# Kernel tuning notes

Measured on AMD Instinct MI355X. Metric: run time of the kernel, lower is better.

Reference implementation:

```python
import jax, jax.numpy as jnp
import numpy as np

B, S, D_IN, D_OUT, H = 4, 2048, 1024, 1024, 16
HD = D_OUT // H  # 64


def setup_inputs() -> dict:
    key = jax.random.key(0)
    ks = jax.random.split(key, 6)
    s = 1.0 / np.sqrt(D_IN)
    return {
        "x": jax.random.normal(ks[0], (B, S, D_IN), dtype=jnp.float32),
        "Wq": jax.random.uniform(ks[1], (D_IN, D_OUT), jnp.float32, -s, s),
        "Wk": jax.random.uniform(ks[2], (D_IN, D_OUT), jnp.float32, -s, s),
        "Wv": jax.random.uniform(ks[3], (D_IN, D_OUT), jnp.float32, -s, s),
        "Wo": jax.random.uniform(ks[4], (D_OUT, D_OUT), jnp.float32, -s, s),
        "bo": jax.random.uniform(ks[5], (D_OUT,), jnp.float32, -s, s),
    }


def reference(x, Wq, Wk, Wv, Wo, bo):
    b, s, _ = x.shape
    # QKV projections -> [b, H, s, hd]
    def split_heads(t):
        return t.reshape(b, s, H, HD).transpose(0, 2, 1, 3)
    q = split_heads(x @ Wq)
    k = split_heads(x @ Wk)
    v = split_heads(x @ Wv)
    # attention scores [b, H, s, s]
    scores = jnp.einsum("bhqd,bhkd->bhqk", q, k)
    causal = jnp.triu(jnp.ones((s, s), dtype=bool), k=1)
    scores = jnp.where(causal, -jnp.inf, scores)
    attn = jax.nn.softmax(scores / np.sqrt(HD), axis=-1)
    ctx = jnp.einsum("bhqk,bhkd->bhqd", attn, v)
    ctx = ctx.transpose(0, 2, 1, 3).reshape(b, s, D_OUT)
    return ctx @ Wo + bo
```

## Files before the change

kernel.cpp:

```cpp
#include <hip/hip_runtime.h>

typedef __attribute__((ext_vector_type(8))) short bf16x8;
typedef __attribute__((ext_vector_type(4))) float f32x4;
typedef __attribute__((ext_vector_type(4))) unsigned uint4v;

#define SM_C 0.18033688011112042f
#define SM_M 20.0f
#define MFMA16 __builtin_amdgcn_mfma_f32_16x16x32_bf16

__device__ __forceinline__ unsigned short f2bf(float f) {
  unsigned u = __builtin_bit_cast(unsigned, f);
  u += 0x7fffu + ((u >> 16) & 1u);
  return (unsigned short)(u >> 16);
}

__device__ __forceinline__ unsigned cvtpk(float lo, float hi) {
  unsigned r;
  asm volatile("v_cvt_pk_bf16_f32 %0, %1, %2" : "=v"(r) : "v"(lo), "v"(hi));
  return r;
}

__device__ __forceinline__ void gload16(const void* g, void* lds) {
  __builtin_amdgcn_global_load_lds(
      (const __attribute__((address_space(1))) void*)g,
      (__attribute__((address_space(3))) void*)lds, 16, 0, 0);
}

#define BARRIER __builtin_amdgcn_s_barrier()
#define LGKM0 asm volatile("s_waitcnt lgkmcnt(0)" ::: "memory")

__global__ __launch_bounds__(256) void cvt_x(const float* __restrict__ in,
                                             unsigned short* __restrict__ out,
                                             int n4) {
  int i = blockIdx.x * 256 + threadIdx.x;
  int stride = gridDim.x * 256;
  for (; i < n4; i += stride) {
    float4 v = ((const float4*)in)[i];
    unsigned short o0 = f2bf(v.x), o1 = f2bf(v.y), o2 = f2bf(v.z), o3 = f2bf(v.w);
    unsigned long long packed = (unsigned long long)o0 | ((unsigned long long)o1 << 16) |
                                ((unsigned long long)o2 << 32) | ((unsigned long long)o3 << 48);
    ((unsigned long long*)out)[i] = packed;
  }
}

__global__ __launch_bounds__(256) void transpose_w4(const float* __restrict__ W0,
                                                    const float* __restrict__ W1,
                                                    const float* __restrict__ W2,
                                                    const float* __restrict__ W3,
                                                    unsigned short* __restrict__ WT) {
  __shared__ float tile[32][33];
  const int z = blockIdx.z;
  const float* W = (z == 0) ? W0 : (z == 1) ? W1 : (z == 2) ? W2 : W3;
  unsigned short* WTo = WT + (size_t)z * 1048576;
  int bx = blockIdx.x, by = blockIdx.y;
  int x = bx * 32 + threadIdx.x;
  for (int i = 0; i < 4; ++i) {
    int r = threadIdx.y + i * 8;
    tile[r][threadIdx.x] = W[(by * 32 + r) * 1024 + x];
  }
  __syncthreads();
  int nx = by * 32 + threadIdx.x;
  for (int i = 0; i < 4; ++i) {
    int r = threadIdx.y + i * 8;
    WTo[(long)(bx * 32 + r) * 1024 + nx] = f2bf(tile[threadIdx.x][r]);
  }
}

template <int NR, int MODE>
__global__ __launch_bounds__(512, 1) void gemm3b(const unsigned short* __restrict__ A,
                                                 const unsigned short* __restrict__ BT,
                                                 unsigned short* __restrict__ Cb,
                                                 float* __restrict__ Cf,
                                                 const float* __restrict__ bias,
                                                 int M, int N, int K) {
  constexpr int BN = NR * 64;
  __shared__ alignas(16) unsigned short As[3][256 * 64];
  __shared__ alignas(16) unsigned short Bs[2][BN * 64];

  const int nbn = N / BN;
  const int tmg = (M / 256) / 8;
  const int cc = blockIdx.x >> 3, xc = blockIdx.x & 7;
  const int tm = xc * tmg + cc / nbn, tn = cc % nbn;

  const int t = threadIdx.x, l = t & 63, wid = t >> 6;
  const int wm = wid >> 2, wn = wid & 3;
  const int lr = l & 15, lg = l >> 4;

  f32x4 acc[8][NR] = {};

  const int sq = t >> 3;
  const int sslot8 = ((t & 7) ^ (sq & 7)) * 8;
  const unsigned short* Ath = A + ((long)tm * 256 + sq) * K + sslot8;
  const unsigned short* Bth = BT + ((long)tn * BN + sq) * K + sslot8;
  const int ldsoff = sq * 64 + (t & 7) * 8;

#define STGA(buf, q, kt) \
  gload16(Ath + (long)((q)*64) * K + (kt)*64, &As[buf][(q)*4096 + ldsoff])
#define STGB(buf, u, kt) \
  gload16(Bth + (long)((u)*64) * K + (kt)*64, &Bs[buf][(u)*4096 + ldsoff])

  const int NT = K >> 6;
#pragma unroll
  for (int q = 0; q < 4; ++q) STGA(0, q, 0);
#pragma unroll
  for (int u = 0; u < NR; ++u) STGB(0, u, 0);
#pragma unroll
  for (int q = 0; q < 4; ++q) STGA(1, q, 1);

  const int offk0 = (lg ^ (lr & 7)) * 8;
  const int offk1 = ((4 + lg) ^ (lr & 7)) * 8;
  const int arow0 = (wm * 128 + lr) * 64;
  const int brow0 = (wn * (NR * 16) + lr) * 64;

#define DS_A(MH)                                                   \
  _Pragma("unroll") for (int m_ = 0; m_ < 4; ++m_) {               \
    const unsigned short* ap_ = Ac + arow0 + ((MH)*4 + m_) * 1024; \
    af[m_][0] = *(const bf16x8*)(ap_ + offk0);                     \
    af[m_][1] = *(const bf16x8*)(ap_ + offk1);                     \
  }
#define DS_B_ALL                                          \
  _Pragma("unroll") for (int n_ = 0; n_ < NR; ++n_) {     \
    const unsigned short* bp_ = Bc + brow0 + n_ * 1024;   \
    bfr[n_][0] = *(const bf16x8*)(bp_ + offk0);           \
    bfr[n_][1] = *(const bf16x8*)(bp_ + offk1);           \
  }
#define MM(MH)                                                              \
  __builtin_amdgcn_s_setprio(1);                                            \
  _Pragma("unroll") for (int m_ = 0; m_ < 4; ++m_)                          \
  _Pragma("unroll") for (int n_ = 0; n_ < NR; ++n_) {                       \
    acc[(MH)*4 + m_][n_] = MFMA16(af[m_][0], bfr[n_][0],                    \
                                  acc[(MH)*4 + m_][n_], 0, 0, 0);           \
    acc[(MH)*4 + m_][n_] = MFMA16(af[m_][1], bfr[n_][1],                    \
                                  acc[(MH)*4 + m_][n_], 0, 0, 0);           \
  }                                                                         \
  __builtin_amdgcn_s_setprio(0);

  int cur3 = 0;
  int stg3 = 2;
  for (int tt = 0; tt < NT; ++tt) {
    const unsigned short* Ac = As[cur3];
    const unsigned short* Bc = Bs[tt & 1];

    bf16x8 af[4][2];
    bf16x8 bfr[NR][2];

    if (tt == NT - 1) asm volatile("s_waitcnt vmcnt(0)" ::: "memory");
    else              asm volatile("s_waitcnt vmcnt(4)" ::: "memory");
    BARRIER;
    DS_A(0);
    DS_B_ALL;
    if (tt + 1 < NT) {
      const int nbB = (tt + 1) & 1;
#pragma unroll
      for (int u = 0; u < NR; ++u) STGB(nbB, u, tt + 1);
    }
    BARRIER;
    LGKM0;
    MM(0);

    DS_A(1);
    if (tt + 2 < NT) {
#pragma unroll
      for (int q = 0; q < 4; ++q) STGA(stg3, q, tt + 2);
    }
    BARRIER;
    LGKM0;
    MM(1);

    cur3 = (cur3 == 2) ? 0 : cur3 + 1;
    stg3 = (stg3 == 2) ? 0 : stg3 + 1;
  }
#undef DS_A
#undef DS_B_ALL
#undef MM
#undef STGA
#undef STGB

  const long crow = (long)tm * 256 + wm * 128;
  const int ccol = tn * BN + wn * (NR * 16);

  if constexpr (MODE == 1) {
#pragma unroll
    for (int m = 0; m < 8; ++m)
#pragma unroll
      for (int n = 0; n < NR; ++n)
#pragma unroll
        for (int r = 0; r < 4; ++r) {
          long row = crow + m * 16 + lg * 4 + r;
          int col = ccol + n * 16 + lr;
          Cf[row * N + col] = acc[m][n][r] + bias[col];
        }
  } else {
#pragma unroll
    for (int n = 0; n < NR; ++n) {
      const int colg = ccol + n * 16;
      const int plane = colg >> 10;
      if (plane < 2) {
        unsigned short* pl = Cb + (size_t)plane * 8388608;
        const int pc = (colg & 1023) + lr;
#pragma unroll
        for (int m = 0; m < 8; ++m)
#pragma unroll
          for (int r = 0; r < 4; ++r) {
            long row = crow + m * 16 + lg * 4 + r;
            pl[row * 1024 + pc] = f2bf(acc[m][n][r]);
          }
      } else {
        unsigned short* VtW = Cb + 16777216;
        const int bq = (tm >> 3) << 4;
        const int sbase = ((tm & 7) << 8) + wm * 128;
        const int vcol = (colg & 1023) + lr;
        const long vtrow = (long)(bq + (vcol >> 6)) * 64 + (vcol & 63);
#pragma unroll
        for (int m = 0; m < 8; ++m) {
          const int srow_ = sbase + m * 16 + lg * 4;
          const int lwb = srow_ & 63;
          const int stt = srow_ >> 6;
          const int vp0 = (lwb & 32) | (((lwb >> 2) & 3) << 3) | (((lwb >> 4) & 1) << 2);
          unsigned long long pk4 =
              (unsigned long long)f2bf(acc[m][n][0]) |
              ((unsigned long long)f2bf(acc[m][n][1]) << 16) |
              ((unsigned long long)f2bf(acc[m][n][2]) << 32) |
              ((unsigned long long)f2bf(acc[m][n][3]) << 48);
          *(unsigned long long*)(VtW + vtrow * 2048 + stt * 64 + vp0) = pk4;
        }
      }
    }
  }
}

template <int TWO>
__device__ __forceinline__ void attn_tile(
    const unsigned short* __restrict__ Kc, const unsigned short* __restrict__ Vc,
    int lr, int lg, bool mask0, bool mask1, int kv0, int q0row, int q1row,
    const bf16x8 (&qf)[2][2], f32x4 (&cacc)[2][4], float (&l_r)[2]) {
  constexpr int S0 = TWO ? 0 : 1;
  f32x4 p[2][4];
#pragma unroll
  for (int s = S0; s < 2; ++s)
#pragma unroll
    for (int g = 0; g < 4; ++g) p[s][g] = f32x4{0.f, 0.f, 0.f, 0.f};

  __builtin_amdgcn_s_setprio(1);
#pragma unroll
  for (int g = 0; g < 4; ++g) {
    const int key = g * 16 + lr;
    const int swz = (key & 7) << 3;
#pragma unroll
    for (int c = 0; c < 2; ++c) {
      bf16x8 kf = *(const bf16x8*)(Kc + key * 64 + ((c * 32 + lg * 8) ^ swz));
#pragma unroll
      for (int s = S0; s < 2; ++s)
        p[s][g] = MFMA16(kf, qf[s][c], p[s][g], 0, 0, 0);
    }
  }
  __builtin_amdgcn_s_setprio(0);

  if (TWO && mask0) {
#pragma unroll
    for (int g = 0; g < 4; ++g)
#pragma unroll
      for (int r = 0; r < 4; ++r)
        if (kv0 + g * 16 + lg * 4 + r > q0row) p[0][g][r] = -1e30f;
  }
  if (mask1) {
#pragma unroll
    for (int g = 0; g < 4; ++g)
#pragma unroll
      for (int r = 0; r < 4; ++r)
        if (kv0 + g * 16 + lg * 4 + r > q1row) p[1][g][r] = -1e30f;
  }

  const float SM_NMC = -SM_M * SM_C;
  unsigned pk[2][4][2];
#pragma unroll
  for (int s = S0; s < 2; ++s) {
    float e[4][4];
#pragma unroll
    for (int g = 0; g < 4; ++g)
#pragma unroll
      for (int r = 0; r < 4; ++r)
        e[g][r] = __builtin_amdgcn_exp2f(__builtin_fmaf(p[s][g][r], SM_C, SM_NMC));
    float t0 = (e[0][0] + e[0][1]) + (e[0][2] + e[0][3]);
    float t1 = (e[1][0] + e[1][1]) + (e[1][2] + e[1][3]);
    float t2 = (e[2][0] + e[2][1]) + (e[2][2] + e[2][3]);
    float t3 = (e[3][0] + e[3][1]) + (e[3][2] + e[3][3]);
    l_r[s] += (t0 + t1) + (t2 + t3);
#pragma unroll
    for (int g = 0; g < 4; ++g) {
      pk[s][g][0] = cvtpk(e[g][0], e[g][1]);
      pk[s][g][1] = cvtpk(e[g][2], e[g][3]);
    }
  }

#pragma unroll
  for (int sl = 0; sl < 2; ++sl) {
    bf16x8 vf[4];
#pragma unroll
    for (int n = 0; n < 4; ++n) {
      const int hd = n * 16 + lr;
      vf[n] = *(const bf16x8*)(Vc + hd * 64 + ((sl * 32 + lg * 8) ^ ((hd & 7) << 3)));
    }
    __builtin_amdgcn_s_setprio(1);
#pragma unroll
    for (int s = S0; s < 2; ++s) {
      uint4v pw = {pk[s][2 * sl][0], pk[s][2 * sl][1], pk[s][2 * sl + 1][0], pk[s][2 * sl + 1][1]};
      bf16x8 pa = __builtin_bit_cast(bf16x8, pw);
#pragma unroll
      for (int n = 0; n < 4; ++n)
        cacc[s][n] = MFMA16(pa, vf[n], cacc[s][n], 0, 0, 0);
    }
    __builtin_amdgcn_s_setprio(0);
  }
}

__global__ __launch_bounds__(256, 4) void flash_attn(const unsigned short* __restrict__ Qp,
                                                     const unsigned short* __restrict__ Kp,
                                                     const unsigned short* __restrict__ Vt,
                                                     unsigned short* __restrict__ Ctx) {
  __shared__ alignas(16) unsigned short Ks[2][64 * 64];
  __shared__ alignas(16) unsigned short Vs[2][64 * 64];
  const int bid = blockIdx.x;
  const int qt = bid >> 6;
  const int bh = bid & 63;
  const int b = bh >> 4, h = bh & 15;
  const int t = threadIdx.x, l = t & 63, w = t >> 6;
  const int lr = l & 15, lg = l >> 4;
  const long rowbase = (long)b * 2048;
  const int colbase = h * 64;
  const int q0 = qt * 64 + w * 16;
  const int q1 = (31 - qt) * 64 + w * 16;
  const int q0row = q0 + lr, q1row = q1 + lr;
  const int nkv = 32 - qt;

  bf16x8 qf[2][2];
#pragma unroll
  for (int c = 0; c < 2; ++c) {
    qf[0][c] = *(const bf16x8*)(Qp + (rowbase + q0 + lr) * 1024 + colbase + c * 32 + lg * 8);
    qf[1][c] = *(const bf16x8*)(Qp + (rowbase + q1 + lr) * 1024 + colbase + c * 32 + lg * 8);
  }

  f32x4 cacc[2][4];
  float l_r[2];
#pragma unroll
  for (int s = 0; s < 2; ++s) {
    l_r[s] = 0.f;
#pragma unroll
    for (int n = 0; n < 4; ++n) cacc[s][n] = f32x4{0.f, 0.f, 0.f, 0.f};
  }

  const int srow = w * 16 + (l >> 3);
  const int scol = (l & 7) * 8;
  const int kswz = scol ^ ((srow & 7) << 3);
  const unsigned short* kp = Kp + (rowbase + srow) * 1024 + colbase + kswz;
  const unsigned short* vp = Vt + ((long)(bh * 64 + srow)) * 2048 + kswz;
  unsigned short* ksd0 = &Ks[0][(w * 16) * 64];
  unsigned short* vsd0 = &Vs[0][(w * 16) * 64];

#define STAGE(buf)                                    \
  do {                                                \
    gload16(kp, ksd0 + (buf) * 4096);                 \
    gload16(kp + 8 * 1024, ksd0 + (buf) * 4096 + 512);\
    gload16(vp, vsd0 + (buf) * 4096);                 \
    gload16(vp + 8 * 2048, vsd0 + (buf) * 4096 + 512);\
    kp += 64 * 1024;                                  \
    vp += 64;                                         \
  } while (0)

#define TILE_WAIT(j)                                                          \
  do {                                                                        \
    if ((j) == nkv - 1) asm volatile("s_waitcnt vmcnt(0)" ::: "memory");      \
    else                asm volatile("s_waitcnt vmcnt(4)" ::: "memory");      \
    asm volatile("s_barrier" ::: "memory");                                   \
  } while (0)

  STAGE(0);
  STAGE(1);

  int j = 0;
  for (; j <= qt; ++j) {
    const int cur = j & 1;
    TILE_WAIT(j);
    attn_tile<1>(Ks[cur], Vs[cur], lr, lg, j == qt, false, j * 64, q0row, q1row,
                 qf, cacc, l_r);
    asm volatile("s_barrier" ::: "memory");
    if (j + 2 < nkv) STAGE(cur);
  }
  for (; j < nkv; ++j) {
    const int cur = j & 1;
    TILE_WAIT(j);
    attn_tile<0>(Ks[cur], Vs[cur], lr, lg, false, j == nkv - 1, j * 64, q0row, q1row,
                 qf, cacc, l_r);
    asm volatile("s_barrier" ::: "memory");
    if (j + 2 < nkv) STAGE(cur);
  }
#undef STAGE
#undef TILE_WAIT

#pragma unroll
  for (int s = 0; s < 2; ++s) {
    float rs = l_r[s];
    rs += __shfl_xor(rs, 16);
    rs += __shfl_xor(rs, 32);
    float invl = 1.f / rs;
    float ilq[4];
#pragma unroll
    for (int r = 0; r < 4; ++r) ilq[r] = __shfl(invl, lg * 20 + r);
    const int qs = (s == 0) ? q0 : q1;
#pragma unroll
    for (int n = 0; n < 4; ++n)
#pragma unroll
      for (int r = 0; r < 4; ++r) {
        long row = rowbase + qs + lg * 4 + r;
        Ctx[row * 1024 + colbase + n * 16 + lr] = f2bf(cacc[s][n][r] * ilq[r]);
      }
  }
}

extern "C" void kernel_launch(void* const* d_in, const int* in_sizes, int n_in,
                              void* d_out, int out_size, void* d_ws, size_t ws_size,
                              hipStream_t stream) {
  (void)in_sizes; (void)n_in; (void)out_size; (void)ws_size;
  const float* x  = (const float*)d_in[0];
  const float* Wq = (const float*)d_in[1];
  const float* Wk = (const float*)d_in[2];
  const float* Wv = (const float*)d_in[3];
  const float* Wo = (const float*)d_in[4];
  const float* bo = (const float*)d_in[5];
  float* out = (float*)d_out;

  unsigned short* ws = (unsigned short*)d_ws;
  unsigned short* xb  = ws;
  unsigned short* WqT = ws + 8388608;
  unsigned short* WoT = WqT + 3145728;
  unsigned short* QKV = WqT + 4194304;
  unsigned short* Qp  = QKV;
  unsigned short* Kp  = QKV + 8388608;
  unsigned short* Vt  = QKV + 16777216;
  unsigned short* Ctx = QKV + 25165824;

  cvt_x<<<2048, 256, 0, stream>>>(x, xb, 8192 * 1024 / 4);

  dim3 tb(32, 8), tg(32, 32, 4);
  transpose_w4<<<tg, tb, 0, stream>>>(Wq, Wk, Wv, Wo, WqT);

  gemm3b<3, 0><<<512, 512, 0, stream>>>(xb, WqT, QKV, nullptr, nullptr,
                                        8192, 3072, 1024);

  flash_attn<<<1024, 256, 0, stream>>>(Qp, Kp, Vt, Ctx);

  gemm3b<2, 1><<<256, 512, 0, stream>>>(Ctx, WoT, nullptr, out, bo,
                                        8192, 1024, 1024);
}
```

Before: 138.6 us.

## Replace 256-row triple-buffered GEMM with 128x128 double-buffered tiles; fuse prep kernels

Merges the x-conversion and weight-transpose kernels into one launch to cut a kernel launch. Replaces the 512-thread 256xBN GEMM that used a 3-stage A buffer and split MFMA phases with a simpler 256-thread 128x128 tile kernel using double buffering and one barrier per k-step. This gives more blocks and higher occupancy, but the smaller tiles mean less data reuse per block. The simpler pipeline also exposes more load latency, since it waits on vmcnt(0) every iteration.

After: 148.3 us, median of 2. 7.0% more time.

```diff
diff --git a/kernel.cpp b/kernel.cpp
--- a/kernel.cpp
+++ b/kernel.cpp
@@ -28,195 +28,174 @@
 
 #define BARRIER __builtin_amdgcn_s_barrier()
 #define LGKM0 asm volatile("s_waitcnt lgkmcnt(0)" ::: "memory")
-
-__global__ __launch_bounds__(256) void cvt_x(const float* __restrict__ in,
-                                             unsigned short* __restrict__ out,
-                                             int n4) {
-  int i = blockIdx.x * 256 + threadIdx.x;
-  int stride = gridDim.x * 256;
-  for (; i < n4; i += stride) {
-    float4 v = ((const float4*)in)[i];
-    unsigned short o0 = f2bf(v.x), o1 = f2bf(v.y), o2 = f2bf(v.z), o3 = f2bf(v.w);
-    unsigned long long packed = (unsigned long long)o0 | ((unsigned long long)o1 << 16) |
-                                ((unsigned long long)o2 << 32) | ((unsigned long long)o3 << 48);
-    ((unsigned long long*)out)[i] = packed;
-  }
-}
-
-__global__ __launch_bounds__(256) void transpose_w4(const float* __restrict__ W0,
-                                                    const float* __restrict__ W1,
-                                                    const float* __restrict__ W2,
-                                                    const float* __restrict__ W3,
-                                                    unsigned short* __restrict__ WT) {
+#define VM0 asm volatile("s_waitcnt vmcnt(0)" ::: "memory")
+
+__global__ __launch_bounds__(256) void prep(const float* __restrict__ x,
+                                            unsigned short* __restrict__ xb,
+                                            const float* __restrict__ W0,
+                                            const float* __restrict__ W1,
+                                            const float* __restrict__ W2,
+                                            const float* __restrict__ W3,
+                                            unsigned short* __restrict__ WT) {
   __shared__ float tile[32][33];
-  const int z = blockIdx.z;
-  const float* W = (z == 0) ? W0 : (z == 1) ? W1 : (z == 2) ? W2 : W3;
-  unsigned short* WTo = WT + (size_t)z * 1048576;
-  int bx = blockIdx.x, by = blockIdx.y;
-  int x = bx * 32 + threadIdx.x;
-  for (int i = 0; i < 4; ++i) {
-    int r = threadIdx.y + i * 8;
-    tile[r][threadIdx.x] = W[(by * 32 + r) * 1024 + x];
-  }
-  __syncthreads();
-  int nx = by * 32 + threadIdx.x;
-  for (int i = 0; i < 4; ++i) {
-    int r = threadIdx.y + i * 8;
-    WTo[(long)(bx * 32 + r) * 1024 + nx] = f2bf(tile[threadIdx.x][r]);
-  }
-}
-
-template <int NR, int MODE>
-__global__ __launch_bounds__(512, 1) void gemm3b(const unsigned short* __restrict__ A,
-                                                 const unsigned short* __restrict__ BT,
-                                                 unsigned short* __restrict__ Cb,
-                                                 float* __restrict__ Cf,
-                                                 const float* __restrict__ bias,
-                                                 int M, int N, int K) {
-  constexpr int BN = NR * 64;
-  __shared__ alignas(16) unsigned short As[3][256 * 64];
-  __shared__ alignas(16) unsigned short Bs[2][BN * 64];
-
-  const int nbn = N / BN;
-  const int tmg = (M / 256) / 8;
+  const int bid = blockIdx.x;
+  if (bid < 2048) {
+    int i = bid * 256 + threadIdx.x;
+    for (; i < 2097152; i += 2048 * 256) {
+      float4 v = ((const float4*)x)[i];
+      unsigned long long packed = (unsigned long long)f2bf(v.x) |
+                                  ((unsigned long long)f2bf(v.y) << 16) |
+                                  ((unsigned long long)f2bf(v.z) << 32) |
+                                  ((unsigned long long)f2bf(v.w) << 48);
+      ((unsigned long long*)xb)[i] = packed;
+    }
+  } else {
+    int b2 = bid - 2048;
+    const int z = b2 >> 10;
+    b2 &= 1023;
+    const int bx = b2 & 31, by = b2 >> 5;
+    const float* W = (z == 0) ? W0 : (z == 1) ? W1 : (z == 2) ? W2 : W3;
+    unsigned short* WTo = WT + (size_t)z * 1048576;
+    const int tx = threadIdx.x & 31, ty = threadIdx.x >> 5;
+    const int xcol = bx * 32 + tx;
+    for (int i = 0; i < 4; ++i) {
+      int r = ty + i * 8;
+      tile[r][tx] = W[(by * 32 + r) * 1024 + xcol];
+    }
+    __syncthreads();
+    const int nx = by * 32 + tx;
+    for (int i = 0; i < 4; ++i) {
+      int r = ty + i * 8;
+      WTo[(long)(bx * 32 + r) * 1024 + nx] = f2bf(tile[tx][r]);
+    }
+  }
+}
+
+template <int MODE>
+__global__ __launch_bounds__(256) void gemm97(const unsigned short* __restrict__ A,
+                                              const unsigned short* __restrict__ BT,
+                                              unsigned short* __restrict__ Cb,
+                                              float* __restrict__ Cf,
+                                              const float* __restrict__ bias,
+                                              int M, int N, int K) {
+  __shared__ alignas(16) unsigned short As[2][128 * 64];
+  __shared__ alignas(16) unsigned short Bs[2][128 * 64];
+
+  const int nbn = N >> 7;
+  const int tmg = (M >> 7) >> 3;
   const int cc = blockIdx.x >> 3, xc = blockIdx.x & 7;
   const int tm = xc * tmg + cc / nbn, tn = cc % nbn;
 
   const int t = threadIdx.x, l = t & 63, wid = t >> 6;
-  const int wm = wid >> 2, wn = wid & 3;
+  const int wm = wid >> 1, wn = wid & 1;
   const int lr = l & 15, lg = l >> 4;
 
-  f32x4 acc[8][NR] = {};
+  f32x4 acc[4][4] = {};
 
   const int sq = t >> 3;
   const int sslot8 = ((t & 7) ^ (sq & 7)) * 8;
-  const unsigned short* Ath = A + ((long)tm * 256 + sq) * K + sslot8;
-  const unsigned short* Bth = BT + ((long)tn * BN + sq) * K + sslot8;
+  const unsigned short* Ath = A + ((long)tm * 128 + sq) * K + sslot8;
+  const unsigned short* Bth = BT + ((long)tn * 128 + sq) * K + sslot8;
   const int ldsoff = sq * 64 + (t & 7) * 8;
 
-#define STGA(buf, q, kt) \
-  gload16(Ath + (long)((q)*64) * K + (kt)*64, &As[buf][(q)*4096 + ldsoff])
-#define STGB(buf, u, kt) \
-  gload16(Bth + (long)((u)*64) * K + (kt)*64, &Bs[buf][(u)*4096 + ldsoff])
+#define STG(buf, kt)                                                      \
+  do {                                                                    \
+    _Pragma("unroll") for (int q_ = 0; q_ < 4; ++q_) {                    \
+      gload16(Ath + (long)(q_ * 32) * K + (kt) * 64,                      \
+              &As[buf][q_ * 2048 + ldsoff]);                              \
+      gload16(Bth + (long)(q_ * 32) * K + (kt) * 64,                      \
+              &Bs[buf][q_ * 2048 + ldsoff]);                              \
+    }                                                                     \
+  } while (0)
 
   const int NT = K >> 6;
-#pragma unroll
-  for (int q = 0; q < 4; ++q) STGA(0, q, 0);
-#pragma unroll
-  for (int u = 0; u < NR; ++u) STGB(0, u, 0);
-#pragma unroll
-  for (int q = 0; q < 4; ++q) STGA(1, q, 1);
+  STG(0, 0);
+  VM0;
+  BARRIER;
 
   const int offk0 = (lg ^ (lr & 7)) * 8;
   const int offk1 = ((4 + lg) ^ (lr & 7)) * 8;
-  const int arow0 = (wm * 128 + lr) * 64;
-  const int brow0 = (wn * (NR * 16) + lr) * 64;
-
-#define DS_A(MH)                                                   \
-  _Pragma("unroll") for (int m_ = 0; m_ < 4; ++m_) {               \
-    const unsigned short* ap_ = Ac + arow0 + ((MH)*4 + m_) * 1024; \
-    af[m_][0] = *(const bf16x8*)(ap_ + offk0);                     \
-    af[m_][1] = *(const bf16x8*)(ap_ + offk1);                     \
-  }
-#define DS_B_ALL                                          \
-  _Pragma("unroll") for (int n_ = 0; n_ < NR; ++n_) {     \
-    const unsigned short* bp_ = Bc + brow0 + n_ * 1024;   \
-    bfr[n_][0] = *(const bf16x8*)(bp_ + offk0);           \
-    bfr[n_][1] = *(const bf16x8*)(bp_ + offk1);           \
-  }
-#define MM(MH)                                                              \
-  __builtin_amdgcn_s_setprio(1);                                            \
-  _Pragma("unroll") for (int m_ = 0; m_ < 4; ++m_)                          \
-  _Pragma("unroll") for (int n_ = 0; n_ < NR; ++n_) {                       \
-    acc[(MH)*4 + m_][n_] = MFMA16(af[m_][0], bfr[n_][0],                    \
-                                  acc[(MH)*4 + m_][n_], 0, 0, 0);           \
-    acc[(MH)*4 + m_][n_] = MFMA16(af[m_][1], bfr[n_][1],                    \
-                                  acc[(MH)*4 + m_][n_], 0, 0, 0);           \
-  }                                                                         \
-  __builtin_amdgcn_s_setprio(0);
-
-  int cur3 = 0;
-  int stg3 = 2;
+  const int arow0 = (wm * 64 + lr) * 64;
+  const int brow0 = (wn * 64 + lr) * 64;
+
   for (int tt = 0; tt < NT; ++tt) {
-    const unsigned short* Ac = As[cur3];
-    const unsigned short* Bc = Bs[tt & 1];
-
-    bf16x8 af[4][2];
-    bf16x8 bfr[NR][2];
-
-    if (tt == NT - 1) asm volatile("s_waitcnt vmcnt(0)" ::: "memory");
-    else              asm volatile("s_waitcnt vmcnt(4)" ::: "memory");
-    BARRIER;
-    DS_A(0);
-    DS_B_ALL;
+    const int cur = tt & 1;
+    if (tt + 1 < NT) STG(cur ^ 1, tt + 1);
+
+    const unsigned short* Ac = As[cur];
+    const unsigned short* Bc = Bs[cur];
+    bf16x8 af[4][2], bfr[4][2];
+#pragma unroll
+    for (int m = 0; m < 4; ++m) {
+      const unsigned short* ap = Ac + arow0 + m * 1024;
+      af[m][0] = *(const bf16x8*)(ap + offk0);
+      af[m][1] = *(const bf16x8*)(ap + offk1);
+    }
+#pragma unroll
+    for (int n = 0; n < 4; ++n) {
+      const unsigned short* bp = Bc + brow0 + n * 1024;
+      bfr[n][0] = *(const bf16x8*)(bp + offk0);
+      bfr[n][1] = *(const bf16x8*)(bp + offk1);
+    }
+    LGKM0;
+    __builtin_amdgcn_s_setprio(1);
+#pragma unroll
+    for (int m = 0; m < 4; ++m)
+#pragma unroll
+      for (int n = 0; n < 4; ++n) {
+        acc[m][n] = MFMA16(af[m][0], bfr[n][0], acc[m][n], 0, 0, 0);
+        acc[m][n] = MFMA16(af[m][1], bfr[n][1], acc[m][n], 0, 0, 0);
+      }
+    __builtin_amdgcn_s_setprio(0);
+
     if (tt + 1 < NT) {
-      const int nbB = (tt + 1) & 1;
-#pragma unroll
-      for (int u = 0; u < NR; ++u) STGB(nbB, u, tt + 1);
-    }
-    BARRIER;
-    LGKM0;
-    MM(0);
-
-    DS_A(1);
-    if (tt + 2 < NT) {
-#pragma unroll
-      for (int q = 0; q < 4; ++q) STGA(stg3, q, tt + 2);
-    }
-    BARRIER;
-    LGKM0;
-    MM(1);
-
-    cur3 = (cur3 == 2) ? 0 : cur3 + 1;
-    stg3 = (stg3 == 2) ? 0 : stg3 + 1;
-  }
-#undef DS_A
-#undef DS_B_ALL
-#undef MM
-#undef STGA
-#undef STGB
-
-  const long crow = (long)tm * 256 + wm * 128;
-  const int ccol = tn * BN + wn * (NR * 16);
+      VM0;
+      BARRIER;
+    }
+  }
+#undef STG
+
+  const long crow = (long)tm * 128 + wm * 64;
+  const int ccolw = wn * 64;
 
   if constexpr (MODE == 1) {
 #pragma unroll
-    for (int m = 0; m < 8; ++m)
-#pragma unroll
-      for (int n = 0; n < NR; ++n)
+    for (int m = 0; m < 4; ++m)
+#pragma unroll
+      for (int n = 0; n < 4; ++n)
 #pragma unroll
         for (int r = 0; r < 4; ++r) {
           long row = crow + m * 16 + lg * 4 + r;
-          int col = ccol + n * 16 + lr;
+          int col = tn * 128 + ccolw + n * 16 + lr;
           Cf[row * N + col] = acc[m][n][r] + bias[col];
         }
   } else {
-#pragma unroll
-    for (int n = 0; n < NR; ++n) {
-      const int colg = ccol + n * 16;
-      const int plane = colg >> 10;
-      if (plane < 2) {
-        unsigned short* pl = Cb + (size_t)plane * 8388608;
-        const int pc = (colg & 1023) + lr;
-#pragma unroll
-        for (int m = 0; m < 8; ++m)
+    if (tn < 16) {
+      unsigned short* pl = Cb + ((tn < 8) ? 0 : 8388608);
+      const int pc = (tn & 7) * 128 + ccolw + lr;
+#pragma unroll
+      for (int m = 0; m < 4; ++m)
+#pragma unroll
+        for (int n = 0; n < 4; ++n)
 #pragma unroll
           for (int r = 0; r < 4; ++r) {
             long row = crow + m * 16 + lg * 4 + r;
-            pl[row * 1024 + pc] = f2bf(acc[m][n][r]);
+            pl[row * 1024 + pc + n * 16] = f2bf(acc[m][n][r]);
           }
-      } else {
-        unsigned short* VtW = Cb + 16777216;
-        const int bq = (tm >> 3) << 4;
-        const int sbase = ((tm & 7) << 8) + wm * 128;
-        const int vcol = (colg & 1023) + lr;
-        const long vtrow = (long)(bq + (vcol >> 6)) * 64 + (vcol & 63);
-#pragma unroll
-        for (int m = 0; m < 8; ++m) {
-          const int srow_ = sbase + m * 16 + lg * 4;
-          const int lwb = srow_ & 63;
-          const int stt = srow_ >> 6;
-          const int vp0 = (lwb & 32) | (((lwb >> 2) & 3) << 3) | (((lwb >> 4) & 1) << 2);
+    } else {
+      unsigned short* VtW = Cb + 16777216;
+      const int bq = (tm >> 4) << 4;
+      const int sbase = ((tm & 15) << 7) + wm * 64;
+#pragma unroll
+      for (int m = 0; m < 4; ++m) {
+        const int srow_ = sbase + m * 16 + lg * 4;
+        const int lwb = srow_ & 63;
+        const int stt = srow_ >> 6;
+        const int vp0 = (lwb & 32) | (((lwb >> 2) & 3) << 3) | (((lwb >> 4) & 1) << 2);
+#pragma unroll
+        for (int n = 0; n < 4; ++n) {
+          const int vcol = (tn - 16) * 128 + ccolw + n * 16 + lr;
+          const long vtrow = (long)(bq + (vcol >> 6)) * 64 + (vcol & 63);
           unsigned long long pk4 =
               (unsigned long long)f2bf(acc[m][n][0]) |
               ((unsigned long long)f2bf(acc[m][n][1]) << 16) |
@@ -439,16 +418,13 @@
   unsigned short* Vt  = QKV + 16777216;
   unsigned short* Ctx = QKV + 25165824;
 
-  cvt_x<<<2048, 256, 0, stream>>>(x, xb, 8192 * 1024 / 4);
-
-  dim3 tb(32, 8), tg(32, 32, 4);
-  transpose_w4<<<tg, tb, 0, stream>>>(Wq, Wk, Wv, Wo, WqT);
-
-  gemm3b<3, 0><<<512, 512, 0, stream>>>(xb, WqT, QKV, nullptr, nullptr,
-                                        8192, 3072, 1024);
+  prep<<<6144, 256, 0, stream>>>(x, xb, Wq, Wk, Wv, Wo, WqT);
+
+  gemm97<0><<<1536, 256, 0, stream>>>(xb, WqT, QKV, nullptr, nullptr,
+                                      8192, 3072, 1024);
 
   flash_attn<<<1024, 256, 0, stream>>>(Qp, Kp, Vt, Ctx);
 
-  gemm3b<2, 1><<<256, 512, 0, stream>>>(Ctx, WoT, nullptr, out, bo,
-                                        8192, 1024, 1024);
-}
+  gemm97<1><<<512, 256, 0, stream>>>(Ctx, WoT, nullptr, out, bo,
+                                     8192, 1024, 1024);
+}
```
